# Optimization experiments

Measured on AMD Instinct MI355X. Metric: run time of the kernel, lower is better.

Reference implementation:

```python
import jax, jax.numpy as jnp
import numpy as np

N_NODES = 100_000
E = 1_600_000
IN_F = 128
H = 64
PROP = 3
EPS = 1e-5


def layer_norm(x, w, b):
    mu = x.mean(-1, keepdims=True)
    var = ((x - mu) ** 2).mean(-1, keepdims=True)
    return (x - mu) * jax.lax.rsqrt(var + EPS) * w + b


def setup_inputs() -> dict:
    key = jax.random.key(0)
    ks = jax.random.split(key, 6)
    in_feat = jax.random.normal(ks[0], (N_NODES, IN_F), dtype=jnp.float32)
    edge_index = jax.random.randint(ks[1], (2, E), 0, N_NODES, dtype=jnp.int32)
    lin_w = jax.random.normal(ks[2], (IN_F, H), dtype=jnp.float32) * (1.0 / np.sqrt(IN_F))
    lin_b = jnp.zeros((H,), jnp.float32)
    conv_w = jax.random.normal(ks[3], (H, H), dtype=jnp.float32) * (1.0 / np.sqrt(H))
    conv_b = jnp.zeros((H,), jnp.float32)
    ln_w = jnp.ones((PROP, H), jnp.float32)
    ln_b = jnp.zeros((PROP, H), jnp.float32)
    return {"in_feat": in_feat, "edge_index": edge_index, "lin_w": lin_w,
            "lin_b": lin_b, "conv_w": conv_w, "conv_b": conv_b,
            "ln_w": ln_w, "ln_b": ln_b}


def reference(in_feat, edge_index, lin_w, lin_b, conv_w, conv_b, ln_w, ln_b):
    n = in_feat.shape[0]
    # GCNConv normalization: add self-loops, symmetric D^-1/2 (A+I) D^-1/2
    loops = jnp.arange(n, dtype=edge_index.dtype)
    src = jnp.concatenate([edge_index[0], loops])
    dst = jnp.concatenate([edge_index[1], loops])
    deg = jax.ops.segment_sum(jnp.ones_like(dst, jnp.float32), dst, num_segments=n)
    dinv = jax.lax.rsqrt(jnp.maximum(deg, 1.0))  # deg >= 1 due to self-loops
    coef = (dinv[src] * dinv[dst])[:, None]      # [E+n, 1]

    def conv(h):
        h = h @ conv_w                             # [N, H]
        agg = jax.ops.segment_sum(h[src] * coef, dst, num_segments=n)
        return agg + conv_b

    h = in_feat @ lin_w + lin_b                    # project in_feats -> h_feats
    ori = h
    for i in range(PROP):
        if i != 0:
            h = h + ori                            # residual (res=True)
            h = layer_norm(h, ln_w[i], ln_b[i])    # norm=True
            h = jax.nn.relu(h)                     # relu=True (dropout=eval identity)
        h = conv(h)                                # shared GCNConv
    return h
```

## Files before the change

kernel.cpp:

```cpp
#include <hip/hip_runtime.h>


static constexpr int NN    = 100000;
static constexpr int NE    = 1600000;
static constexpr int HF    = 64;
static constexpr int NNP   = 100352;
static constexpr int NBUK  = 391;
static constexpr int PBLK  = 512;
static constexpr int CHUNK = NE / PBLK;
static constexpr int SCN   = NBUK * PBLK;
static constexpr int GB    = SCN / 256;
#define EPSV 1e-5f

static __device__ __forceinline__ unsigned short f2bf(float f) {
    unsigned u = __float_as_uint(f);
    u = (u + 0x7FFFu + ((u >> 16) & 1u)) >> 16;
    return (unsigned short)u;
}

__global__ __launch_bounds__(256) void k_bhist(const int* __restrict__ ei,
                                               int* __restrict__ bh) {
    __shared__ int cnts[NBUK];
    for (int b = threadIdx.x; b < NBUK; b += 256) cnts[b] = 0;
    __syncthreads();
    int base = blockIdx.x * CHUNK;
    for (int k = threadIdx.x; k < CHUNK; k += 256)
        atomicAdd(&cnts[ei[NE + base + k] >> 8], 1);
    __syncthreads();
    for (int b = threadIdx.x; b < NBUK; b += 256)
        bh[blockIdx.x * NBUK + b] = cnts[b];
}

__global__ __launch_bounds__(256) void k_scan1g(const int* __restrict__ bh,
                                                int* __restrict__ offs,
                                                int* __restrict__ bsum) {
    __shared__ int sm[256];
    int i = blockIdx.x * 256 + threadIdx.x;
    int buk = i >> 9, blk = i & (PBLK - 1);
    int x = bh[blk * NBUK + buk];
    sm[threadIdx.x] = x;
    __syncthreads();
    int v = x;
    for (int off = 1; off < 256; off <<= 1) {
        int t = (threadIdx.x >= (unsigned)off) ? sm[threadIdx.x - off] : 0;
        __syncthreads();
        v += t;
        sm[threadIdx.x] = v;
        __syncthreads();
    }
    offs[i] = v - x;
    if (threadIdx.x == 255) bsum[blockIdx.x] = v;
}

__global__ __launch_bounds__(1024) void k_scan2g(int* __restrict__ bsum, int nb) {
    __shared__ int sm[1024];
    int t = threadIdx.x;
    int x = (t < nb) ? bsum[t] : 0;
    sm[t] = x;
    __syncthreads();
    int v = x;
    for (int off = 1; off < 1024; off <<= 1) {
        int tt = (t >= off) ? sm[t - off] : 0;
        __syncthreads();
        v += tt;
        sm[t] = v;
        __syncthreads();
    }
    if (t < nb) bsum[t] = v - x;
}

__global__ __launch_bounds__(256) void k_scan3g(int* __restrict__ offs,
                                                const int* __restrict__ bsum) {
    int i = blockIdx.x * 256 + threadIdx.x;
    offs[i] += bsum[blockIdx.x];
}

__global__ __launch_bounds__(256) void k_part(const int* __restrict__ ei,
                                              const int* __restrict__ offs,
                                              unsigned* __restrict__ part) {
    __shared__ int cur[NBUK];
    int blk = blockIdx.x;
    for (int b = threadIdx.x; b < NBUK; b += 256) cur[b] = offs[b * PBLK + blk];
    __syncthreads();
    int base = blk * CHUNK;
    for (int k = threadIdx.x; k < CHUNK; k += 256) {
        int s = ei[base + k];
        int d = ei[NE + base + k];
        int pos = atomicAdd(&cur[d >> 8], 1);
        part[pos] = (unsigned)s | ((unsigned)(d & 255) << 17);
    }
}

__global__ __launch_bounds__(256) void k_fineA(const unsigned* __restrict__ part,
                                               const int* __restrict__ offs,
                                               int* __restrict__ rowp,
                                               float* __restrict__ dinv) {
    __shared__ int cnt[256];
    __shared__ int sm[256];
    int b = blockIdx.x;
    int row0 = b << 8;
    cnt[threadIdx.x] = 0;
    __syncthreads();
    int bstart = offs[b * PBLK];
    int bend   = (b == NBUK - 1) ? NE : offs[(b + 1) * PBLK];
    for (int k = bstart + threadIdx.x; k < bend; k += 256)
        atomicAdd(&cnt[part[k] >> 17], 1);
    __syncthreads();
    int x = cnt[threadIdx.x];
    sm[threadIdx.x] = x;
    __syncthreads();
    int v = x;
    for (int off = 1; off < 256; off <<= 1) {
        int t = (threadIdx.x >= (unsigned)off) ? sm[threadIdx.x - off] : 0;
        __syncthreads();
        v += t;
        sm[threadIdx.x] = v;
        __syncthreads();
    }
    int row = row0 + threadIdx.x;
    if (row < NN) {
        rowp[row] = bstart + v - x;
        dinv[row] = rsqrtf((float)x + 1.0f);
    }
    if (row == NN - 1 || (b == NBUK - 1 && threadIdx.x == 255))
        rowp[NN] = NE;
}

__global__ __launch_bounds__(256) void k_fineB(const unsigned* __restrict__ part,
                                               const int* __restrict__ rowp,
                                               const int* __restrict__ offs,
                                               const float* __restrict__ dinv,
                                               uint2* __restrict__ es2) {
    __shared__ int   cur[256];
    __shared__ float dlo[256];
    int b = blockIdx.x;
    int row0 = b << 8;
    int row = row0 + threadIdx.x;
    if (row < NN) {
        cur[threadIdx.x] = rowp[row];
        dlo[threadIdx.x] = dinv[row];
    } else {
        cur[threadIdx.x] = 0;
        dlo[threadIdx.x] = 0.0f;
    }
    __syncthreads();
    int bstart = offs[b * PBLK];
    int bend   = (b == NBUK - 1) ? NE : offs[(b + 1) * PBLK];
    for (int k = bstart + threadIdx.x; k < bend; k += 256) {
        unsigned p = part[k];
        int s  = (int)(p & 0x1FFFF);
        int dl = (int)(p >> 17);
        float c = dinv[s] * dlo[dl];
        int pos = atomicAdd(&cur[dl], 1);
        es2[pos] = make_uint2(p & 0x1FFFF, __float_as_uint(c));
    }
}

template<int K, bool DUAL, bool BIAS, bool OUTBF>
__global__ __launch_bounds__(256) void k_gemm(const float* __restrict__ A,
                                              const float* __restrict__ W,
                                              const float* __restrict__ bias,
                                              void* __restrict__ out0v,
                                              float* __restrict__ out1)
{
    __shared__ float As[64][65];
    __shared__ float Ws[64][64];
    const int tid = threadIdx.x;
    const int tx = tid & 15, ty = tid >> 4;
    const int c0 = tx * 4, r0 = ty * 4;
    const int row0 = blockIdx.x * 64;
    float acc[4][4] = {};

    for (int kt = 0; kt < K / 64; ++kt) {
        #pragma unroll
        for (int q = 0; q < 4; ++q) {
            int vid = q * 256 + tid;
            int row = vid >> 4;
            int kq  = vid & 15;
            if (row0 + row < NN) {
                float4 v = *reinterpret_cast<const float4*>(
                    &A[(size_t)(row0 + row) * K + kt * 64 + kq * 4]);
                As[row][kq * 4 + 0] = v.x; As[row][kq * 4 + 1] = v.y;
                As[row][kq * 4 + 2] = v.z; As[row][kq * 4 + 3] = v.w;
            }
            *reinterpret_cast<float4*>(&Ws[row][kq * 4]) =
                *reinterpret_cast<const float4*>(&W[(size_t)(kt * 64 + row) * HF + kq * 4]);
        }
        __syncthreads();
        #pragma unroll 8
        for (int k = 0; k < 64; ++k) {
            float4 wv = *reinterpret_cast<const float4*>(&Ws[k][c0]);
            float a0 = As[r0 + 0][k], a1 = As[r0 + 1][k];
            float a2 = As[r0 + 2][k], a3 = As[r0 + 3][k];
            acc[0][0] += a0 * wv.x; acc[0][1] += a0 * wv.y; acc[0][2] += a0 * wv.z; acc[0][3] += a0 * wv.w;
            acc[1][0] += a1 * wv.x; acc[1][1] += a1 * wv.y; acc[1][2] += a1 * wv.z; acc[1][3] += a1 * wv.w;
            acc[2][0] += a2 * wv.x; acc[2][1] += a2 * wv.y; acc[2][2] += a2 * wv.z; acc[2][3] += a2 * wv.w;
            acc[3][0] += a3 * wv.x; acc[3][1] += a3 * wv.y; acc[3][2] += a3 * wv.z; acc[3][3] += a3 * wv.w;
        }
        __syncthreads();
    }

    float4 bv = make_float4(0.f, 0.f, 0.f, 0.f);
    if (BIAS) bv = *reinterpret_cast<const float4*>(&bias[c0]);
    #pragma unroll
    for (int i = 0; i < 4; ++i) {
        int r = row0 + r0 + i;
        if (r < NN) {
            float4 o = make_float4(acc[i][0] + bv.x, acc[i][1] + bv.y,
                                   acc[i][2] + bv.z, acc[i][3] + bv.w);
            if (OUTBF) {
                ushort4 ob;
                ob.x = f2bf(o.x); ob.y = f2bf(o.y);
                ob.z = f2bf(o.z); ob.w = f2bf(o.w);
                *reinterpret_cast<ushort4*>(
                    &((unsigned short*)out0v)[(size_t)r * HF + c0]) = ob;
            } else {
                *reinterpret_cast<float4*>(&((float*)out0v)[(size_t)r * HF + c0]) = o;
                if (DUAL)
                    *reinterpret_cast<float4*>(&out1[(size_t)r * HF + c0]) = o;
            }
        }
    }
}

template<int FUSE_LN>
__global__ __launch_bounds__(256) void k_gather3(const int* __restrict__ rowp,
                                                 const uint2* __restrict__ es2,
                                                 const float* __restrict__ dinv,
                                                 const unsigned* __restrict__ hwu,
                                                 const float* __restrict__ cb,
                                                 const float* __restrict__ ori,
                                                 const float* __restrict__ lnw,
                                                 const float* __restrict__ lnb,
                                                 float* __restrict__ out)
{
    int row = blockIdx.x * 4 + (threadIdx.x >> 6);
    if (row >= NN) return;
    const int lane = threadIdx.x & 63;
    const int half = lane >> 5;
    const int c2   = lane & 31;
    const float dd = dinv[row];

    float ax, ay;
    if (half == 0) {
        unsigned u = hwu[(size_t)row * 32 + c2];
        float2 cbv = reinterpret_cast<const float2*>(cb)[c2];
        float s2 = dd * dd;
        ax = fmaf(__uint_as_float(u << 16),        s2, cbv.x);
        ay = fmaf(__uint_as_float(u & 0xFFFF0000u), s2, cbv.y);
    } else {
        ax = 0.0f; ay = 0.0f;
    }

    const int start = rowp[row], end = rowp[row + 1];
    for (int base = start; base < end; base += 64) {
        int n = end - base;
        if (n > 64) n = 64;
        int   sl = 0;
        float cl = 0.0f;
        if (lane < n) {
            uint2 p = es2[base + lane];
            sl = (int)p.x;
            cl = __uint_as_float(p.y);
        }
        int j = 0;
        for (; j + 16 <= n; j += 16) {
            int   s0 = __shfl(sl, j +  0 + half), s1 = __shfl(sl, j +  2 + half);
            int   s2_ = __shfl(sl, j +  4 + half), s3 = __shfl(sl, j +  6 + half);
            int   s4 = __shfl(sl, j +  8 + half), s5 = __shfl(sl, j + 10 + half);
            int   s6 = __shfl(sl, j + 12 + half), s7 = __shfl(sl, j + 14 + half);
            float c0 = __shfl(cl, j +  0 + half), c1 = __shfl(cl, j +  2 + half);
            float c2_ = __shfl(cl, j +  4 + half), c3 = __shfl(cl, j +  6 + half);
            float c4 = __shfl(cl, j +  8 + half), c5 = __shfl(cl, j + 10 + half);
            float c6 = __shfl(cl, j + 12 + half), c7 = __shfl(cl, j + 14 + half);
            unsigned u0 = hwu[(size_t)s0 * 32 + c2];
            unsigned u1 = hwu[(size_t)s1 * 32 + c2];
            unsigned u2 = hwu[(size_t)s2_ * 32 + c2];
            unsigned u3 = hwu[(size_t)s3 * 32 + c2];
            unsigned u4 = hwu[(size_t)s4 * 32 + c2];
            unsigned u5 = hwu[(size_t)s5 * 32 + c2];
            unsigned u6 = hwu[(size_t)s6 * 32 + c2];
            unsigned u7 = hwu[(size_t)s7 * 32 + c2];
            ax += __uint_as_float(u0 << 16) * c0;  ay += __uint_as_float(u0 & 0xFFFF0000u) * c0;
            ax += __uint_as_float(u1 << 16) * c1;  ay += __uint_as_float(u1 & 0xFFFF0000u) * c1;
            ax += __uint_as_float(u2 << 16) * c2_; ay += __uint_as_float(u2 & 0xFFFF0000u) * c2_;
            ax += __uint_as_float(u3 << 16) * c3;  ay += __uint_as_float(u3 & 0xFFFF0000u) * c3;
            ax += __uint_as_float(u4 << 16) * c4;  ay += __uint_as_float(u4 & 0xFFFF0000u) * c4;
            ax += __uint_as_float(u5 << 16) * c5;  ay += __uint_as_float(u5 & 0xFFFF0000u) * c5;
            ax += __uint_as_float(u6 << 16) * c6;  ay += __uint_as_float(u6 & 0xFFFF0000u) * c6;
            ax += __uint_as_float(u7 << 16) * c7;  ay += __uint_as_float(u7 & 0xFFFF0000u) * c7;
        }
        for (; j < n; j += 2) {
            int   s = __shfl(sl, j + half);
            float c = __shfl(cl, j + half);
            unsigned u = hwu[(size_t)s * 32 + c2];
            ax += __uint_as_float(u << 16) * c;
            ay += __uint_as_float(u & 0xFFFF0000u) * c;
        }
    }

    ax += __shfl_xor(ax, 32);
    ay += __shfl_xor(ay, 32);

    if (FUSE_LN) {
        float2 o = reinterpret_cast<const float2*>(ori)[(size_t)row * 32 + c2];
        float v0 = ax + o.x, v1 = ay + o.y;
        float s = v0 + v1;
        #pragma unroll
        for (int off = 16; off > 0; off >>= 1) s += __shfl_xor(s, off);
        float mu = s * (1.0f / 64.0f);
        float d0 = v0 - mu, d1 = v1 - mu;
        float q = d0 * d0 + d1 * d1;
        #pragma unroll
        for (int off = 16; off > 0; off >>= 1) q += __shfl_xor(q, off);
        float r = rsqrtf(q * (1.0f / 64.0f) + EPSV);
        float2 wv = reinterpret_cast<const float2*>(lnw)[c2];
        float2 bv = reinterpret_cast<const float2*>(lnb)[c2];
        if (half == 0) {
            float y0 = fmaxf(d0 * r * wv.x + bv.x, 0.0f);
            float y1 = fmaxf(d1 * r * wv.y + bv.y, 0.0f);
            reinterpret_cast<float2*>(out)[(size_t)row * 32 + c2] = make_float2(y0, y1);
        }
    } else {
        if (half == 0)
            reinterpret_cast<float2*>(out)[(size_t)row * 32 + c2] = make_float2(ax, ay);
    }
}

extern "C" void kernel_launch(void* const* d_in, const int* in_sizes, int n_in,
                              void* d_out, int out_size, void* d_ws, size_t ws_size,
                              hipStream_t stream)
{
    const float* in_feat = (const float*)d_in[0];
    const int*   ei      = (const int*)d_in[1];
    const float* lin_w   = (const float*)d_in[2];
    const float* lin_b   = (const float*)d_in[3];
    const float* conv_w  = (const float*)d_in[4];
    const float* conv_b  = (const float*)d_in[5];
    const float* ln_w    = (const float*)d_in[6];
    const float* ln_b    = (const float*)d_in[7];
    float* out = (float*)d_out;
    float* ws  = (float*)d_ws;

    float*    dinv = ws;
    int*      rowp = (int*)(ws + NNP);
    int*      bh   = rowp + NNP;
    int*      offs = bh + SCN;
    int*      bsum = offs + SCN;
    unsigned* part = (unsigned*)(bsum + 1024);
    uint2*    es2  = (uint2*)(part + NE);
    float*    h    = (float*)(es2 + NE);
    float*    ori  = h + (size_t)NN * HF;
    unsigned short* hw16 = (unsigned short*)(ori + (size_t)NN * HF);
    unsigned* hwu  = (unsigned*)hw16;

    k_bhist<<<PBLK, 256, 0, stream>>>(ei, bh);
    k_scan1g<<<GB, 256, 0, stream>>>(bh, offs, bsum);
    k_scan2g<<<1, 1024, 0, stream>>>(bsum, GB);
    k_scan3g<<<GB, 256, 0, stream>>>(offs, bsum);
    k_part<<<PBLK, 256, 0, stream>>>(ei, offs, part);
    k_fineA<<<NBUK, 256, 0, stream>>>(part, offs, rowp, dinv);
    k_fineB<<<NBUK, 256, 0, stream>>>(part, rowp, offs, dinv, es2);

    k_gemm<128, true, true, false><<<(NN + 63) / 64, 256, 0, stream>>>(
        in_feat, lin_w, lin_b, h, ori);

    for (int it = 0; it < 3; ++it) {
        k_gemm<64, false, false, true><<<(NN + 63) / 64, 256, 0, stream>>>(
            h, conv_w, nullptr, hw16, nullptr);
        if (it < 2) {
            k_gather3<1><<<(NN + 3) / 4, 256, 0, stream>>>(
                rowp, es2, dinv, hwu, conv_b, ori,
                ln_w + (it + 1) * HF, ln_b + (it + 1) * HF, h);
        } else {
            k_gather3<0><<<(NN + 3) / 4, 256, 0, stream>>>(
                rowp, es2, dinv, hwu, conv_b, nullptr, nullptr, nullptr, out);
        }
    }
}
```

Before: 423.1 us.

## Store intermediates in bf16, fold scan fixup, use 32-lane gather rows

Stores the projected features h, the residual ori, and the post-LayerNorm activations in bf16 instead of fp32. The conv GEMM now reads bf16 input, which halves intermediate memory traffic. The separate scan-fixup kernel is removed and the block-sum add is folded into its consumers, saving one launch. The gather kernel now assigns 32 lanes per row with 8 rows per block, instead of 64 lanes split into two halves followed by a cross-half reduction. Keeping the residual and LN output in bf16 costs extra rounding error on top of the existing bf16 hw storage.

```diff
diff --git a/kernel.cpp b/kernel.cpp
--- a/kernel.cpp
+++ b/kernel.cpp
@@ -17,6 +17,12 @@
     u = (u + 0x7FFFu + ((u >> 16) & 1u)) >> 16;
     return (unsigned short)u;
 }
+static __device__ __forceinline__ float bf_lo(unsigned u) {
+    return __uint_as_float(u << 16);
+}
+static __device__ __forceinline__ float bf_hi(unsigned u) {
+    return __uint_as_float(u & 0xFFFF0000u);
+}
 
 __global__ __launch_bounds__(256) void k_bhist(const int* __restrict__ ei,
                                                int* __restrict__ bh) {
@@ -69,18 +75,16 @@
     if (t < nb) bsum[t] = v - x;
 }
 
-__global__ __launch_bounds__(256) void k_scan3g(int* __restrict__ offs,
-                                                const int* __restrict__ bsum) {
-    int i = blockIdx.x * 256 + threadIdx.x;
-    offs[i] += bsum[blockIdx.x];
-}
-
 __global__ __launch_bounds__(256) void k_part(const int* __restrict__ ei,
                                               const int* __restrict__ offs,
+                                              const int* __restrict__ bsum,
                                               unsigned* __restrict__ part) {
     __shared__ int cur[NBUK];
     int blk = blockIdx.x;
-    for (int b = threadIdx.x; b < NBUK; b += 256) cur[b] = offs[b * PBLK + blk];
+    for (int b = threadIdx.x; b < NBUK; b += 256) {
+        int i = b * PBLK + blk;
+        cur[b] = offs[i] + bsum[i >> 8];
+    }
     __syncthreads();
     int base = blk * CHUNK;
     for (int k = threadIdx.x; k < CHUNK; k += 256) {
@@ -93,6 +97,7 @@
 
 __global__ __launch_bounds__(256) void k_fineA(const unsigned* __restrict__ part,
                                                const int* __restrict__ offs,
+                                               const int* __restrict__ bsum,
                                                int* __restrict__ rowp,
                                                float* __restrict__ dinv) {
     __shared__ int cnt[256];
@@ -101,8 +106,11 @@
     int row0 = b << 8;
     cnt[threadIdx.x] = 0;
     __syncthreads();
-    int bstart = offs[b * PBLK];
-    int bend   = (b == NBUK - 1) ? NE : offs[(b + 1) * PBLK];
+    int i0 = b * PBLK;
+    int bstart = offs[i0] + bsum[i0 >> 8];
+    int bend;
+    if (b == NBUK - 1) bend = NE;
+    else { int i1 = (b + 1) * PBLK; bend = offs[i1] + bsum[i1 >> 8]; }
     for (int k = bstart + threadIdx.x; k < bend; k += 256)
         atomicAdd(&cnt[part[k] >> 17], 1);
     __syncthreads();
@@ -122,13 +130,13 @@
         rowp[row] = bstart + v - x;
         dinv[row] = rsqrtf((float)x + 1.0f);
     }
-    if (row == NN - 1 || (b == NBUK - 1 && threadIdx.x == 255))
-        rowp[NN] = NE;
+    if (row == NN - 1) rowp[NN] = NE;
 }
 
 __global__ __launch_bounds__(256) void k_fineB(const unsigned* __restrict__ part,
                                                const int* __restrict__ rowp,
                                                const int* __restrict__ offs,
+                                               const int* __restrict__ bsum,
                                                const float* __restrict__ dinv,
                                                uint2* __restrict__ es2) {
     __shared__ int   cur[256];
@@ -144,24 +152,26 @@
         dlo[threadIdx.x] = 0.0f;
     }
     __syncthreads();
-    int bstart = offs[b * PBLK];
-    int bend   = (b == NBUK - 1) ? NE : offs[(b + 1) * PBLK];
+    int i0 = b * PBLK;
+    int bstart = offs[i0] + bsum[i0 >> 8];
+    int bend;
+    if (b == NBUK - 1) bend = NE;
+    else { int i1 = (b + 1) * PBLK; bend = offs[i1] + bsum[i1 >> 8]; }
     for (int k = bstart + threadIdx.x; k < bend; k += 256) {
         unsigned p = part[k];
         int s  = (int)(p & 0x1FFFF);
         int dl = (int)(p >> 17);
         float c = dinv[s] * dlo[dl];
         int pos = atomicAdd(&cur[dl], 1);
-        es2[pos] = make_uint2(p & 0x1FFFF, __float_as_uint(c));
-    }
-}
-
-template<int K, bool DUAL, bool BIAS, bool OUTBF>
-__global__ __launch_bounds__(256) void k_gemm(const float* __restrict__ A,
-                                              const float* __restrict__ W,
-                                              const float* __restrict__ bias,
-                                              void* __restrict__ out0v,
-                                              float* __restrict__ out1)
+        es2[pos] = make_uint2((unsigned)s, __float_as_uint(c));
+    }
+}
+
+__global__ __launch_bounds__(256) void k_gemmA(const float* __restrict__ A,
+                                               const float* __restrict__ W,
+                                               const float* __restrict__ bias,
+                                               unsigned short* __restrict__ h16,
+                                               unsigned short* __restrict__ ori16)
 {
     __shared__ float As[64][65];
     __shared__ float Ws[64][64];
@@ -171,7 +181,7 @@
     const int row0 = blockIdx.x * 64;
     float acc[4][4] = {};
 
-    for (int kt = 0; kt < K / 64; ++kt) {
+    for (int kt = 0; kt < 2; ++kt) {
         #pragma unroll
         for (int q = 0; q < 4; ++q) {
             int vid = q * 256 + tid;
@@ -179,7 +189,7 @@
             int kq  = vid & 15;
             if (row0 + row < NN) {
                 float4 v = *reinterpret_cast<const float4*>(
-                    &A[(size_t)(row0 + row) * K + kt * 64 + kq * 4]);
+                    &A[(size_t)(row0 + row) * 128 + kt * 64 + kq * 4]);
                 As[row][kq * 4 + 0] = v.x; As[row][kq * 4 + 1] = v.y;
                 As[row][kq * 4 + 2] = v.z; As[row][kq * 4 + 3] = v.w;
             }
@@ -200,130 +210,147 @@
         __syncthreads();
     }
 
-    float4 bv = make_float4(0.f, 0.f, 0.f, 0.f);
-    if (BIAS) bv = *reinterpret_cast<const float4*>(&bias[c0]);
+    float4 bv = *reinterpret_cast<const float4*>(&bias[c0]);
     #pragma unroll
     for (int i = 0; i < 4; ++i) {
         int r = row0 + r0 + i;
         if (r < NN) {
-            float4 o = make_float4(acc[i][0] + bv.x, acc[i][1] + bv.y,
-                                   acc[i][2] + bv.z, acc[i][3] + bv.w);
-            if (OUTBF) {
-                ushort4 ob;
-                ob.x = f2bf(o.x); ob.y = f2bf(o.y);
-                ob.z = f2bf(o.z); ob.w = f2bf(o.w);
-                *reinterpret_cast<ushort4*>(
-                    &((unsigned short*)out0v)[(size_t)r * HF + c0]) = ob;
-            } else {
-                *reinterpret_cast<float4*>(&((float*)out0v)[(size_t)r * HF + c0]) = o;
-                if (DUAL)
-                    *reinterpret_cast<float4*>(&out1[(size_t)r * HF + c0]) = o;
-            }
+            ushort4 ob;
+            ob.x = f2bf(acc[i][0] + bv.x); ob.y = f2bf(acc[i][1] + bv.y);
+            ob.z = f2bf(acc[i][2] + bv.z); ob.w = f2bf(acc[i][3] + bv.w);
+            *reinterpret_cast<ushort4*>(&h16[(size_t)r * HF + c0])   = ob;
+            *reinterpret_cast<ushort4*>(&ori16[(size_t)r * HF + c0]) = ob;
+        }
+    }
+}
+
+__global__ __launch_bounds__(256) void k_gemmB(const unsigned* __restrict__ h16u,
+                                               const float* __restrict__ W,
+                                               unsigned short* __restrict__ hw16)
+{
+    __shared__ float As[64][65];
+    __shared__ float Ws[64][64];
+    const int tid = threadIdx.x;
+    const int tx = tid & 15, ty = tid >> 4;
+    const int c0 = tx * 4, r0 = ty * 4;
+    const int row0 = blockIdx.x * 64;
+    float acc[4][4] = {};
+
+    #pragma unroll
+    for (int q = 0; q < 4; ++q) {
+        int vid = q * 256 + tid;
+        int row = vid >> 4;
+        int kq  = vid & 15;
+        if (row0 + row < NN) {
+            uint2 v = *reinterpret_cast<const uint2*>(
+                &h16u[(size_t)(row0 + row) * 32 + kq * 2]);
+            As[row][kq * 4 + 0] = bf_lo(v.x); As[row][kq * 4 + 1] = bf_hi(v.x);
+            As[row][kq * 4 + 2] = bf_lo(v.y); As[row][kq * 4 + 3] = bf_hi(v.y);
+        }
+        *reinterpret_cast<float4*>(&Ws[row][kq * 4]) =
+            *reinterpret_cast<const float4*>(&W[(size_t)row * HF + kq * 4]);
+    }
+    __syncthreads();
+    #pragma unroll 8
+    for (int k = 0; k < 64; ++k) {
+        float4 wv = *reinterpret_cast<const float4*>(&Ws[k][c0]);
+        float a0 = As[r0 + 0][k], a1 = As[r0 + 1][k];
+        float a2 = As[r0 + 2][k], a3 = As[r0 + 3][k];
+        acc[0][0] += a0 * wv.x; acc[0][1] += a0 * wv.y; acc[0][2] += a0 * wv.z; acc[0][3] += a0 * wv.w;
+        acc[1][0] += a1 * wv.x; acc[1][1] += a1 * wv.y; acc[1][2] += a1 * wv.z; acc[1][3] += a1 * wv.w;
+        acc[2][0] += a2 * wv.x; acc[2][1] += a2 * wv.y; acc[2][2] += a2 * wv.z; acc[2][3] += a2 * wv.w;
+        acc[3][0] += a3 * wv.x; acc[3][1] += a3 * wv.y; acc[3][2] += a3 * wv.z; acc[3][3] += a3 * wv.w;
+    }
+
+    #pragma unroll
+    for (int i = 0; i < 4; ++i) {
+        int r = row0 + r0 + i;
+        if (r < NN) {
+            ushort4 ob;
+            ob.x = f2bf(acc[i][0]); ob.y = f2bf(acc[i][1]);
+            ob.z = f2bf(acc[i][2]); ob.w = f2bf(acc[i][3]);
+            *reinterpret_cast<ushort4*>(&hw16[(size_t)r * HF + c0]) = ob;
         }
     }
 }
 
 template<int FUSE_LN>
-__global__ __launch_bounds__(256) void k_gather3(const int* __restrict__ rowp,
+__global__ __launch_bounds__(256) void k_gather4(const int* __restrict__ rowp,
                                                  const uint2* __restrict__ es2,
                                                  const float* __restrict__ dinv,
                                                  const unsigned* __restrict__ hwu,
                                                  const float* __restrict__ cb,
-                                                 const float* __restrict__ ori,
+                                                 const unsigned* __restrict__ ori16,
                                                  const float* __restrict__ lnw,
                                                  const float* __restrict__ lnb,
-                                                 float* __restrict__ out)
+                                                 void* __restrict__ outv)
 {
-    int row = blockIdx.x * 4 + (threadIdx.x >> 6);
+    int row = blockIdx.x * 8 + (threadIdx.x >> 5);
     if (row >= NN) return;
-    const int lane = threadIdx.x & 63;
-    const int half = lane >> 5;
-    const int c2   = lane & 31;
+    const int c2 = threadIdx.x & 31;
     const float dd = dinv[row];
 
-    float ax, ay;
-    if (half == 0) {
-        unsigned u = hwu[(size_t)row * 32 + c2];
-        float2 cbv = reinterpret_cast<const float2*>(cb)[c2];
-        float s2 = dd * dd;
-        ax = fmaf(__uint_as_float(u << 16),        s2, cbv.x);
-        ay = fmaf(__uint_as_float(u & 0xFFFF0000u), s2, cbv.y);
-    } else {
-        ax = 0.0f; ay = 0.0f;
-    }
+    unsigned su = hwu[(size_t)row * 32 + c2];
+    float2 cbv = reinterpret_cast<const float2*>(cb)[c2];
+    float s2 = dd * dd;
+    float ax = fmaf(bf_lo(su), s2, cbv.x);
+    float ay = fmaf(bf_hi(su), s2, cbv.y);
 
     const int start = rowp[row], end = rowp[row + 1];
-    for (int base = start; base < end; base += 64) {
+    for (int base = start; base < end; base += 32) {
         int n = end - base;
-        if (n > 64) n = 64;
+        if (n > 32) n = 32;
         int   sl = 0;
         float cl = 0.0f;
-        if (lane < n) {
-            uint2 p = es2[base + lane];
+        if (c2 < n) {
+            uint2 p = es2[base + c2];
             sl = (int)p.x;
             cl = __uint_as_float(p.y);
         }
         int j = 0;
-        for (; j + 16 <= n; j += 16) {
-            int   s0 = __shfl(sl, j +  0 + half), s1 = __shfl(sl, j +  2 + half);
-            int   s2_ = __shfl(sl, j +  4 + half), s3 = __shfl(sl, j +  6 + half);
-            int   s4 = __shfl(sl, j +  8 + half), s5 = __shfl(sl, j + 10 + half);
-            int   s6 = __shfl(sl, j + 12 + half), s7 = __shfl(sl, j + 14 + half);
-            float c0 = __shfl(cl, j +  0 + half), c1 = __shfl(cl, j +  2 + half);
-            float c2_ = __shfl(cl, j +  4 + half), c3 = __shfl(cl, j +  6 + half);
-            float c4 = __shfl(cl, j +  8 + half), c5 = __shfl(cl, j + 10 + half);
-            float c6 = __shfl(cl, j + 12 + half), c7 = __shfl(cl, j + 14 + half);
-            unsigned u0 = hwu[(size_t)s0 * 32 + c2];
-            unsigned u1 = hwu[(size_t)s1 * 32 + c2];
-            unsigned u2 = hwu[(size_t)s2_ * 32 + c2];
-            unsigned u3 = hwu[(size_t)s3 * 32 + c2];
-            unsigned u4 = hwu[(size_t)s4 * 32 + c2];
-            unsigned u5 = hwu[(size_t)s5 * 32 + c2];
-            unsigned u6 = hwu[(size_t)s6 * 32 + c2];
-            unsigned u7 = hwu[(size_t)s7 * 32 + c2];
-            ax += __uint_as_float(u0 << 16) * c0;  ay += __uint_as_float(u0 & 0xFFFF0000u) * c0;
-            ax += __uint_as_float(u1 << 16) * c1;  ay += __uint_as_float(u1 & 0xFFFF0000u) * c1;
-            ax += __uint_as_float(u2 << 16) * c2_; ay += __uint_as_float(u2 & 0xFFFF0000u) * c2_;
-            ax += __uint_as_float(u3 << 16) * c3;  ay += __uint_as_float(u3 & 0xFFFF0000u) * c3;
-            ax += __uint_as_float(u4 << 16) * c4;  ay += __uint_as_float(u4 & 0xFFFF0000u) * c4;
-            ax += __uint_as_float(u5 << 16) * c5;  ay += __uint_as_float(u5 & 0xFFFF0000u) * c5;
-            ax += __uint_as_float(u6 << 16) * c6;  ay += __uint_as_float(u6 & 0xFFFF0000u) * c6;
-            ax += __uint_as_float(u7 << 16) * c7;  ay += __uint_as_float(u7 & 0xFFFF0000u) * c7;
-        }
-        for (; j < n; j += 2) {
-            int   s = __shfl(sl, j + half);
-            float c = __shfl(cl, j + half);
+        for (; j + 8 <= n; j += 8) {
+            unsigned uu[8]; float cc[8];
+            #pragma unroll
+            for (int q = 0; q < 8; ++q) {
+                int s = __shfl(sl, j + q, 32);
+                cc[q] = __shfl(cl, j + q, 32);
+                uu[q] = hwu[(size_t)s * 32 + c2];
+            }
+            #pragma unroll
+            for (int q = 0; q < 8; ++q) {
+                ax += bf_lo(uu[q]) * cc[q];
+                ay += bf_hi(uu[q]) * cc[q];
+            }
+        }
+        for (; j < n; ++j) {
+            int   s = __shfl(sl, j, 32);
+            float c = __shfl(cl, j, 32);
             unsigned u = hwu[(size_t)s * 32 + c2];
-            ax += __uint_as_float(u << 16) * c;
-            ay += __uint_as_float(u & 0xFFFF0000u) * c;
-        }
-    }
-
-    ax += __shfl_xor(ax, 32);
-    ay += __shfl_xor(ay, 32);
+            ax += bf_lo(u) * c;
+            ay += bf_hi(u) * c;
+        }
+    }
 
     if (FUSE_LN) {
-        float2 o = reinterpret_cast<const float2*>(ori)[(size_t)row * 32 + c2];
-        float v0 = ax + o.x, v1 = ay + o.y;
+        unsigned uo = ori16[(size_t)row * 32 + c2];
+        float v0 = ax + bf_lo(uo), v1 = ay + bf_hi(uo);
         float s = v0 + v1;
         #pragma unroll
-        for (int off = 16; off > 0; off >>= 1) s += __shfl_xor(s, off);
+        for (int off = 16; off > 0; off >>= 1) s += __shfl_xor(s, off, 32);
         float mu = s * (1.0f / 64.0f);
         float d0 = v0 - mu, d1 = v1 - mu;
-        float q = d0 * d0 + d1 * d1;
+        float q2 = d0 * d0 + d1 * d1;
         #pragma unroll
-        for (int off = 16; off > 0; off >>= 1) q += __shfl_xor(q, off);
-        float r = rsqrtf(q * (1.0f / 64.0f) + EPSV);
+        for (int off = 16; off > 0; off >>= 1) q2 += __shfl_xor(q2, off, 32);
+        float r = rsqrtf(q2 * (1.0f / 64.0f) + EPSV);
         float2 wv = reinterpret_cast<const float2*>(lnw)[c2];
         float2 bv = reinterpret_cast<const float2*>(lnb)[c2];
-        if (half == 0) {
-            float y0 = fmaxf(d0 * r * wv.x + bv.x, 0.0f);
-            float y1 = fmaxf(d1 * r * wv.y + bv.y, 0.0f);
-            reinterpret_cast<float2*>(out)[(size_t)row * 32 + c2] = make_float2(y0, y1);
-        }
+        float y0 = fmaxf(fmaf(d0 * r, wv.x, bv.x), 0.0f);
+        float y1 = fmaxf(fmaf(d1 * r, wv.y, bv.y), 0.0f);
+        ((unsigned*)outv)[(size_t)row * 32 + c2] =
+            (unsigned)f2bf(y0) | ((unsigned)f2bf(y1) << 16);
     } else {
-        if (half == 0)
-            reinterpret_cast<float2*>(out)[(size_t)row * 32 + c2] = make_float2(ax, ay);
+        reinterpret_cast<float2*>(outv)[(size_t)row * 32 + c2] = make_float2(ax, ay);
     }
 }
 
@@ -349,31 +376,30 @@
     int*      bsum = offs + SCN;
     unsigned* part = (unsigned*)(bsum + 1024);
     uint2*    es2  = (uint2*)(part + NE);
-    float*    h    = (float*)(es2 + NE);
-    float*    ori  = h + (size_t)NN * HF;
-    unsigned short* hw16 = (unsigned short*)(ori + (size_t)NN * HF);
-    unsigned* hwu  = (unsigned*)hw16;
+    unsigned short* h16  = (unsigned short*)(es2 + NE);
+    unsigned short* ori16 = h16 + (size_t)NN * HF;
+    unsigned short* hw16  = ori16 + (size_t)NN * HF;
+    unsigned* h16u  = (unsigned*)h16;
+    unsigned* ori16u = (unsigned*)ori16;
+    unsigned* hwu   = (unsigned*)hw16;
 
     k_bhist<<<PBLK, 256, 0, stream>>>(ei, bh);
     k_scan1g<<<GB, 256, 0, stream>>>(bh, offs, bsum);
     k_scan2g<<<1, 1024, 0, stream>>>(bsum, GB);
-    k_scan3g<<<GB, 256, 0, stream>>>(offs, bsum);
-    k_part<<<PBLK, 256, 0, stream>>>(ei, offs, part);
-    k_fineA<<<NBUK, 256, 0, stream>>>(part, offs, rowp, dinv);
-    k_fineB<<<NBUK, 256, 0, stream>>>(part, rowp, offs, dinv, es2);
-
-    k_gemm<128, true, true, false><<<(NN + 63) / 64, 256, 0, stream>>>(
-        in_feat, lin_w, lin_b, h, ori);
+    k_part<<<PBLK, 256, 0, stream>>>(ei, offs, bsum, part);
+    k_fineA<<<NBUK, 256, 0, stream>>>(part, offs, bsum, rowp, dinv);
+    k_fineB<<<NBUK, 256, 0, stream>>>(part, rowp, offs, bsum, dinv, es2);
+
+    k_gemmA<<<(NN + 63) / 64, 256, 0, stream>>>(in_feat, lin_w, lin_b, h16, ori16);
 
     for (int it = 0; it < 3; ++it) {
-        k_gemm<64, false, false, true><<<(NN + 63) / 64, 256, 0, stream>>>(
-            h, conv_w, nullptr, hw16, nullptr);
+        k_gemmB<<<(NN + 63) / 64, 256, 0, stream>>>(h16u, conv_w, hw16);
         if (it < 2) {
-            k_gather3<1><<<(NN + 3) / 4, 256, 0, stream>>>(
-                rowp, es2, dinv, hwu, conv_b, ori,
-                ln_w + (it + 1) * HF, ln_b + (it + 1) * HF, h);
+            k_gather4<1><<<(NN + 7) / 8, 256, 0, stream>>>(
+                rowp, es2, dinv, hwu, conv_b, ori16u,
+                ln_w + (it + 1) * HF, ln_b + (it + 1) * HF, h16u);
         } else {
-            k_gather3<0><<<(NN + 3) / 4, 256, 0, stream>>>(
+            k_gather4<0><<<(NN + 7) / 8, 256, 0, stream>>>(
                 rowp, es2, dinv, hwu, conv_b, nullptr, nullptr, nullptr, out);
         }
     }
```

After: 360.6 us. 1.17x faster.
